# Kernel tuning notes

Hardware: AMD Instinct MI355X
Metric: run time of the kernel (lower is better)

## Reference

```python
import jax, jax.numpy as jnp
import numpy as np

D_MODEL = 1024
N_HEADS = 16
HEAD_DIM = D_MODEL // N_HEADS
B, S = 2, 2048


def setup_inputs() -> dict:
    key = jax.random.key(0)
    ks = jax.random.split(key, 6)
    w_scale = 1.0 / np.sqrt(D_MODEL)
    return {
        "query": jax.random.normal(ks[0], (B, S, D_MODEL), dtype=jnp.float32),
        "Wq": jax.random.normal(ks[1], (D_MODEL, D_MODEL), dtype=jnp.float32) * w_scale,
        "Wk": jax.random.normal(ks[2], (D_MODEL, D_MODEL), dtype=jnp.float32) * w_scale,
        "Wv": jax.random.normal(ks[3], (D_MODEL, D_MODEL), dtype=jnp.float32) * w_scale,
        "Wo": jax.random.normal(ks[4], (D_MODEL, D_MODEL), dtype=jnp.float32) * w_scale,
        "bo": jnp.zeros((D_MODEL,), dtype=jnp.float32),
    }


def reference(query, Wq, Wk, Wv, Wo, bo):
    # Self-attention: key = value = query (forward() defaults).
    b, t, _ = query.shape
    # Q/K/V projections (nn.Linear applies x @ W.T; weights here are stored as
    # [out, in] like torch, so project with W.T). Split into heads: [B,H,T,Dh].
    def proj(x, W):
        return (x @ W.T).reshape(b, t, N_HEADS, HEAD_DIM).transpose(0, 2, 1, 3)

    q = proj(query, Wq)
    k = proj(query, Wk)
    v = proj(query, Wv)

    scale = 1.0 / np.sqrt(HEAD_DIM)
    scores = jnp.einsum("bhqd,bhkd->bhqk", q, k) * scale  # [B,H,T,T]
    # Causal mask (is_causal=True, not cross-attention).
    causal = jnp.tril(jnp.ones((t, t), dtype=bool))
    scores = jnp.where(causal, scores, jnp.finfo(scores.dtype).min)
    weights = jax.nn.softmax(scores, axis=-1)
    out = jnp.einsum("bhqk,bhkd->bhqd", weights, v)  # [B,H,T,Dh]
    out = out.transpose(0, 2, 1, 3).reshape(b, t, D_MODEL)
    # Output projection with bias (dropout is identity in eval mode).
    return out @ Wo.T + bo
```

## Files before the change

### kernel.cpp

```cpp
#include <hip/hip_runtime.h>
#include <hip/hip_bf16.h>
#include <math.h>

typedef __attribute__((ext_vector_type(8))) short short8;
typedef __attribute__((ext_vector_type(4))) float floatx4;
typedef __attribute__((ext_vector_type(2))) _Float16 half2v;
typedef __attribute__((ext_vector_type(4))) _Float16 half4v;

#define MFMA_BF16_32(a, b, c) __builtin_amdgcn_mfma_f32_16x16x32_bf16(a, b, c, 0, 0, 0)
#define MFMA_F16_16(a, b, c) __builtin_amdgcn_mfma_f32_16x16x16f16(a, b, c, 0, 0, 0)

#define PIPE_BAR2() asm volatile("s_waitcnt vmcnt(2)\n\ts_barrier" ::: "memory")
#define PIPE_BAR0() asm volatile("s_waitcnt vmcnt(0)\n\ts_barrier" ::: "memory")

static constexpr int NH = 16;
static constexpr int Bb = 2;
static constexpr int Ss = 2048;
static constexpr int DM = 1024;

__device__ inline unsigned short f2bf(float f) {
    unsigned int u = __float_as_uint(f);
    u += 0x7fffu + ((u >> 16) & 1u);
    return (unsigned short)(u >> 16);
}

__device__ __forceinline__ half2v pkrtz(float a, float b) {
    return __builtin_bit_cast(half2v, __builtin_amdgcn_cvt_pkrtz(a, b));
}

__device__ __forceinline__ void gload_lds16(const unsigned short* g, unsigned short* l) {
    __builtin_amdgcn_global_load_lds(
        (const __attribute__((address_space(1))) unsigned int*)g,
        (__attribute__((address_space(3))) unsigned int*)l, 16, 0, 0);
}

__global__ void convert_all(const float* __restrict__ X, const float* __restrict__ w0,
                            const float* __restrict__ w1, const float* __restrict__ w2,
                            const float* __restrict__ w3, unsigned short* __restrict__ dstX,
                            unsigned short* __restrict__ dstW) {
    const int bid = blockIdx.x;
    const float* src;
    unsigned short* dst;
    int i;
    if (bid < 4096) {
        src = X; dst = dstX; i = bid * 256 + threadIdx.x;
    } else {
        const int w = (bid - 4096) >> 10;
        src = (w == 0) ? w0 : (w == 1) ? w1 : (w == 2) ? w2 : w3;
        dst = dstW + (size_t)w * 1048576;
        i = ((bid - 4096) & 1023) * 256 + threadIdx.x;
    }
    float4 v = ((const float4*)src)[i];
    ushort4 o;
    o.x = f2bf(v.x); o.y = f2bf(v.y); o.z = f2bf(v.z); o.w = f2bf(v.w);
    ((ushort4*)dst)[i] = o;
}

__global__ __launch_bounds__(256, 6) void gemm_qkv(const unsigned short* __restrict__ A,
                                                   const unsigned short* __restrict__ W,
                                                   unsigned short* __restrict__ Qp,
                                                   unsigned short* __restrict__ Kp,
                                                   unsigned short* __restrict__ Vt) {
    __shared__ __align__(16) unsigned short S[2][6144];
    const int K = 1024;
    const int tid = threadIdx.x;
    const int wave = tid >> 6, lane = tid & 63;
    const int quad = lane >> 4, l16 = lane & 15;
    const int wr = wave >> 1, wc = wave & 1;

    const int lin = blockIdx.x;
    const int xcd = lin & 7, slot = lin >> 3;
    const int bxt = (xcd & 3) * 16 + (slot & 15);
    const int by = (xcd >> 2) * 12 + (slot >> 4);
    const int bm = bxt * 64;
    const int bn = by * 128;

    const int srow = tid >> 2;
    const int scg = (tid & 3) ^ ((srow >> 1) & 3);
    const unsigned short* gA0 = A + (size_t)(bm + srow) * K + scg * 8;
    const unsigned short* gB0 = W + (size_t)(bn + srow) * K + scg * 8;

    auto stage = [&](int k0, int buf) {
        gload_lds16(gA0 + k0, &S[buf][wave * 512]);
        gload_lds16(gB0 + k0, &S[buf][2048 + wave * 512]);
        gload_lds16(gB0 + (size_t)64 * K + k0, &S[buf][4096 + wave * 512]);
    };

    floatx4 acc[2][4];
#pragma unroll
    for (int i = 0; i < 2; i++)
#pragma unroll
        for (int j = 0; j < 4; j++) acc[i][j] = (floatx4)0.0f;

    stage(0, 0);
    int buf = 0;
    for (int k0 = 0; k0 < K; k0 += 32) {
        __syncthreads();
        if (k0 + 32 < K) stage(k0 + 32, buf ^ 1);
        short8 af[2];
#pragma unroll
        for (int im = 0; im < 2; im++) {
            const int frow = wr * 32 + im * 16 + l16;
            af[im] = *(const short8*)&S[buf][frow * 32 + ((quad ^ ((frow >> 1) & 3)) * 8)];
        }
#pragma unroll
        for (int jn = 0; jn < 4; jn++) {
            const int frow = wc * 64 + jn * 16 + l16;
            short8 bf = *(const short8*)&S[buf][2048 + frow * 32 +
                                               ((quad ^ ((frow >> 1) & 3)) * 8)];
#pragma unroll
            for (int im = 0; im < 2; im++) acc[im][jn] = MFMA_BF16_32(af[im], bf, acc[im][jn]);
        }
        buf ^= 1;
    }
    __syncthreads();

    if (by < 16) {
        unsigned short* LB = &S[0][0];
        unsigned short* dst = (by < 8) ? Qp : Kp;
        const int nb = (by & 7) * 128;
        const float scale = (by < 8) ? 0.125f : 1.0f;
#pragma unroll
        for (int im = 0; im < 2; im++)
#pragma unroll
            for (int jn = 0; jn < 4; jn++) {
                const int row = wr * 32 + im * 16 + quad * 4;
                const int col = wc * 64 + jn * 16 + l16;
#pragma unroll
                for (int r = 0; r < 4; r++)
                    LB[(row + r) * 132 + col] = f2bf(acc[im][jn][r] * scale);
            }
        __syncthreads();
#pragma unroll
        for (int i = 0; i < 4; ++i) {
            const int flat = i * 256 + tid;
            const int row = flat >> 4, ch = flat & 15;
            short8 v = *(const short8*)&LB[row * 132 + ch * 8];
            *(short8*)&dst[(size_t)(bm + row) * 1024 + nb + ch * 8] = v;
        }
    } else {
        _Float16* LF = (_Float16*)&S[0][0];
        const int dbase = (by - 16) * 128;
        const int bI = bm >> 11, sbase = bm & 2047;
#pragma unroll
        for (int im = 0; im < 2; im++)
#pragma unroll
            for (int jn = 0; jn < 4; jn++) {
                const int d = wc * 64 + jn * 16 + l16;
                const int sl = wr * 32 + im * 16 + quad * 4;
                *(half2v*)&LF[d * 66 + sl] = pkrtz(acc[im][jn][0], acc[im][jn][1]);
                *(half2v*)&LF[d * 66 + sl + 2] = pkrtz(acc[im][jn][2], acc[im][jn][3]);
            }
        __syncthreads();
#pragma unroll
        for (int i = 0; i < 4; ++i) {
            const int flat = i * 256 + tid;
            const int dr = flat >> 3, ch = flat & 7;
            short8 v = *(const short8*)&LF[dr * 66 + ch * 8];
            const int d = dbase + dr;
            const int head = d >> 6, d64 = d & 63;
            *(short8*)&Vt[(((size_t)(bI * 16 + head)) * 64 + d64) * 2048 + sbase + ch * 8] = v;
        }
    }
}

__global__ __launch_bounds__(256) void gemm_out(const unsigned short* __restrict__ A,
                                                const unsigned short* __restrict__ Bm,
                                                float* __restrict__ C,
                                                const float* __restrict__ bias) {
    __shared__ __align__(16) unsigned short As[2][8192];
    __shared__ __align__(16) unsigned short Bs[2][4096];
    const int K = 1024;
    const int tid = threadIdx.x;
    const int wave = tid >> 6, lane = tid & 63;
    const int quad = lane >> 4, l16 = lane & 15;

    const int l = blockIdx.x;
    const int xcd = l & 7, slot = l >> 3;
    const int bx = (xcd & 3) * 8 + (slot & 7);
    const int by = (xcd >> 2) * 8 + (slot >> 3);
    const int bm = bx * 128, bn = by * 64;

    const int s0 = wave * 64 + lane;
    const int srow = s0 >> 2;
    const int scg = (s0 & 3) ^ ((srow >> 1) & 3);
    const unsigned short* gA0 = A + (size_t)(bm + srow) * K + scg * 8;
    const unsigned short* gB0 = Bm + (size_t)(bn + srow) * K + scg * 8;

    auto stage = [&](int k0, int buf) {
#pragma unroll
        for (int kh = 0; kh < 2; ++kh) {
            gload_lds16(gA0 + k0 + kh * 32, &As[buf][kh * 4096 + wave * 512]);
            gload_lds16(gA0 + (size_t)64 * K + k0 + kh * 32,
                        &As[buf][kh * 4096 + 2048 + wave * 512]);
            gload_lds16(gB0 + k0 + kh * 32, &Bs[buf][kh * 2048 + wave * 512]);
        }
    };

    floatx4 acc[2][4];
#pragma unroll
    for (int i = 0; i < 2; i++)
#pragma unroll
        for (int j = 0; j < 4; j++) acc[i][j] = (floatx4)0.0f;

    stage(0, 0);
    int buf = 0;
    for (int k0 = 0; k0 < K; k0 += 64) {
        __syncthreads();
        if (k0 + 64 < K) stage(k0 + 64, buf ^ 1);
#pragma unroll
        for (int kh = 0; kh < 2; ++kh) {
            const int abase = kh * 4096, bbase = kh * 2048;
            short8 af[2];
#pragma unroll
            for (int im = 0; im < 2; im++) {
                const int frow = wave * 32 + im * 16 + l16;
                af[im] = *(const short8*)&As[buf][abase + frow * 32 +
                                                  ((quad ^ ((frow >> 1) & 3)) * 8)];
            }
#pragma unroll
            for (int jn = 0; jn < 4; jn++) {
                const int frow = jn * 16 + l16;
                short8 bf = *(const short8*)&Bs[buf][bbase + frow * 32 +
                                                     ((quad ^ ((frow >> 1) & 3)) * 8)];
#pragma unroll
                for (int im = 0; im < 2; im++) acc[im][jn] = MFMA_BF16_32(af[im], bf, acc[im][jn]);
            }
        }
        buf ^= 1;
    }

#pragma unroll
    for (int im = 0; im < 2; im++) {
#pragma unroll
        for (int jn = 0; jn < 4; jn++) {
            const int row0 = bm + wave * 32 + im * 16 + quad * 4;
            const int colg = bn + jn * 16 + l16;
            const float bv = bias[colg];
#pragma unroll
            for (int r = 0; r < 4; r++)
                C[(size_t)(row0 + r) * 1024 + colg] = acc[im][jn][r] + bv;
        }
    }
}

__global__ __launch_bounds__(512, 4) void flash_attn(const unsigned short* __restrict__ Qp,
                                                     const unsigned short* __restrict__ Kp,
                                                     const _Float16* __restrict__ Vt,
                                                     unsigned short* __restrict__ Out) {
    __shared__ __align__(16) unsigned short Ks[3][4096];
    __shared__ __align__(16) _Float16 Vs[3][4096];
    const int lin = blockIdx.x;
    const int xcd = lin & 7, slot = lin >> 3;
    const int pair = xcd * 4 + ((slot >> 4) & 3);
    const int h = pair & 15, b = pair >> 4;
    const int qt0 = slot & 15;
    const int qt = ((slot >> 5) & 1) ? 15 - qt0 : qt0;

    const int tid = threadIdx.x, w = tid >> 6, lane = tid & 63;
    const int quad = lane >> 4, l16 = lane & 15;

    short8 qf[2];
    {
        const unsigned short* qa =
            Qp + ((size_t)(b * 2048 + qt * 128 + w * 16 + l16) << 10) + h * 64 + quad * 8;
        qf[0] = *(const short8*)qa;
        qf[1] = *(const short8*)(qa + 32);
    }

    const int t8 = tid >> 3;
    const int cg = (tid & 7) ^ (t8 & 7);
    const unsigned short* gK0 = Kp + ((size_t)(b * 2048 + t8) << 10) + h * 64 + cg * 8;
    const _Float16* gV0 = Vt + ((size_t)((b * 16 + h) * 64 + t8) << 11) + cg * 8;
    unsigned short* ldsK = &Ks[0][0] + w * 512;
    _Float16* ldsV = &Vs[0][0] + w * 512;

    auto stage = [&](int kt, int buf) {
        const size_t ko = (size_t)kt << 16;
        const size_t vo = (size_t)kt << 6;
        gload_lds16(gK0 + ko, ldsK + buf * 4096);
        gload_lds16((const unsigned short*)(gV0 + vo), (unsigned short*)(ldsV + buf * 4096));
    };

    const int ktEnd = 2 * qt + 1;
    const int myEnd = 2 * qt + (w >> 2);
    stage(0, 0);
    stage(1, 1);

    floatx4 acc[4];
#pragma unroll
    for (int dt = 0; dt < 4; dt++) acc[dt] = (floatx4)0.0f;
    float lsum = 0.0f;
    const int qloc = (w & 3) * 16 + l16;
    const int sw = l16 & 7;

    int buf = 0;
    for (int kt = 0; kt <= ktEnd; ++kt) {
        if (kt < ktEnd) { PIPE_BAR2(); } else { PIPE_BAR0(); }
        const int nbuf = (buf == 2) ? 0 : buf + 1;
        const int pbuf = (nbuf == 2) ? 0 : nbuf + 1;
        if (kt + 2 <= ktEnd) stage(kt + 2, pbuf);
        if (kt <= myEnd) {
            const bool diag = (kt == myEnd);
            const int scMax = diag ? (w & 3) : 3;
            const unsigned short* KB = &Ks[buf][0];
            const _Float16* VB = &Vs[buf][0];

#pragma unroll
            for (int sc = 0; sc < 4; ++sc) {
                if (sc <= scMax) {
                    const int rowk = sc * 16 + l16;
                    short8 kf0 = *(const short8*)&KB[rowk * 64 + ((quad ^ sw) * 8)];
                    short8 kf1 = *(const short8*)&KB[rowk * 64 + (((4 + quad) ^ sw) * 8)];

                    floatx4 s = MFMA_BF16_32(kf0, qf[0], (floatx4)(-2.0f));
                    s = MFMA_BF16_32(kf1, qf[1], s);
                    float ps[4];
#pragma unroll
                    for (int r = 0; r < 4; ++r) {
                        float e = __expf(s[r]);
                        if (diag && (sc * 16 + quad * 4 + r > qloc)) e = 0.0f;
                        ps[r] = e;
                    }
                    lsum += (ps[0] + ps[1]) + (ps[2] + ps[3]);
                    half4v p = __builtin_shufflevector(pkrtz(ps[0], ps[1]),
                                                       pkrtz(ps[2], ps[3]), 0, 1, 2, 3);

#pragma unroll
                    for (int dt = 0; dt < 4; ++dt) {
                        const int rowv = dt * 16 + l16;
                        const int cgv = ((sc * 2 + (quad >> 1)) ^ sw);
                        half4v vf = *(const half4v*)&VB[rowv * 64 + cgv * 8 + (quad & 1) * 4];
                        acc[dt] = MFMA_F16_16(vf, p, acc[dt]);
                    }
                }
            }
        }
        buf = nbuf;
    }

    lsum += __shfl_xor(lsum, 16);
    lsum += __shfl_xor(lsum, 32);
    const float inv = 1.0f / lsum;

    const size_t row = (size_t)(b * 2048 + qt * 128 + w * 16 + l16);
#pragma unroll
    for (int dt = 0; dt < 4; ++dt) {
        const int col = h * 64 + dt * 16 + quad * 4;
        ushort4 o;
        o.x = f2bf(acc[dt][0] * inv);
        o.y = f2bf(acc[dt][1] * inv);
        o.z = f2bf(acc[dt][2] * inv);
        o.w = f2bf(acc[dt][3] * inv);
        *(ushort4*)&Out[row * 1024 + col] = o;
    }
}

extern "C" void kernel_launch(void* const* d_in, const int* in_sizes, int n_in,
                              void* d_out, int out_size, void* d_ws, size_t ws_size,
                              hipStream_t stream) {
    const float* X  = (const float*)d_in[0];
    const float* Wq = (const float*)d_in[1];
    const float* Wk = (const float*)d_in[2];
    const float* Wv = (const float*)d_in[3];
    const float* Wo = (const float*)d_in[4];
    const float* bo = (const float*)d_in[5];

    unsigned short* ws = (unsigned short*)d_ws;
    unsigned short* Xb   = ws;
    unsigned short* W4   = ws + (size_t)4194304;
    unsigned short* Wob  = W4 + (size_t)3145728;
    unsigned short* Qp   = ws + (size_t)8388608;
    unsigned short* Kp   = ws + (size_t)12582912;
    unsigned short* Vt   = ws + (size_t)16777216;
    unsigned short* At   = ws + (size_t)20971520;

    convert_all<<<8192, 256, 0, stream>>>(X, Wq, Wk, Wv, Wo, Xb, W4);

    gemm_qkv<<<1536, 256, 0, stream>>>(Xb, W4, Qp, Kp, Vt);

    flash_attn<<<512, 512, 0, stream>>>(Qp, Kp, (const _Float16*)Vt, At);

    gemm_out<<<512, 256, 0, stream>>>(At, Wob, (float*)d_out, bo);
}
```

Measured before the change: 182.9 us.

## Triple-buffer QKV and output GEMM loads with two-stage-ahead prefetch

Both GEMM kernels move from double-buffered LDS staging to a three-buffer ring that prefetches two k-steps ahead. A fine-grained s_waitcnt vmcnt(3) plus barrier replaces __syncthreads, so one stage of loads can stay in flight while the current tile is consumed. gemm_out also drops its K-step from 64 to 32 so its shared-memory footprint stays bounded, and its occupancy hint is set to 4. The aim is to hide global-load latency better, at the cost of more LDS per block and a lower occupancy target for gemm_qkv (6 to 4).

Measured after the change: 184.8 us. No clear change (+1.0%).

```diff
diff --git a/kernel.cpp b/kernel.cpp
--- a/kernel.cpp
+++ b/kernel.cpp
@@ -12,6 +12,8 @@
 
 #define PIPE_BAR2() asm volatile("s_waitcnt vmcnt(2)\n\ts_barrier" ::: "memory")
 #define PIPE_BAR0() asm volatile("s_waitcnt vmcnt(0)\n\ts_barrier" ::: "memory")
+#define GEMM_BAR3() asm volatile("s_waitcnt vmcnt(3) lgkmcnt(0)\n\ts_barrier" ::: "memory")
+#define GEMM_BAR0() asm volatile("s_waitcnt vmcnt(0) lgkmcnt(0)\n\ts_barrier" ::: "memory")
 
 static constexpr int NH = 16;
 static constexpr int Bb = 2;
@@ -56,12 +58,12 @@
     ((ushort4*)dst)[i] = o;
 }
 
-__global__ __launch_bounds__(256, 6) void gemm_qkv(const unsigned short* __restrict__ A,
+__global__ __launch_bounds__(256, 4) void gemm_qkv(const unsigned short* __restrict__ A,
                                                    const unsigned short* __restrict__ W,
                                                    unsigned short* __restrict__ Qp,
                                                    unsigned short* __restrict__ Kp,
                                                    unsigned short* __restrict__ Vt) {
-    __shared__ __align__(16) unsigned short S[2][6144];
+    __shared__ __align__(16) unsigned short S[3][6144];
     const int K = 1024;
     const int tid = threadIdx.x;
     const int wave = tid >> 6, lane = tid & 63;
@@ -93,10 +95,13 @@
         for (int j = 0; j < 4; j++) acc[i][j] = (floatx4)0.0f;
 
     stage(0, 0);
+    stage(32, 1);
     int buf = 0;
     for (int k0 = 0; k0 < K; k0 += 32) {
-        __syncthreads();
-        if (k0 + 32 < K) stage(k0 + 32, buf ^ 1);
+        if (k0 + 32 < K) { GEMM_BAR3(); } else { GEMM_BAR0(); }
+        const int nbuf = (buf == 2) ? 0 : buf + 1;
+        const int pbuf = (nbuf == 2) ? 0 : nbuf + 1;
+        if (k0 + 64 < K) stage(k0 + 64, pbuf);
         short8 af[2];
 #pragma unroll
         for (int im = 0; im < 2; im++) {
@@ -111,7 +116,7 @@
 #pragma unroll
             for (int im = 0; im < 2; im++) acc[im][jn] = MFMA_BF16_32(af[im], bf, acc[im][jn]);
         }
-        buf ^= 1;
+        buf = nbuf;
     }
     __syncthreads();
 
@@ -164,12 +169,12 @@
     }
 }
 
-__global__ __launch_bounds__(256) void gemm_out(const unsigned short* __restrict__ A,
-                                                const unsigned short* __restrict__ Bm,
-                                                float* __restrict__ C,
-                                                const float* __restrict__ bias) {
-    __shared__ __align__(16) unsigned short As[2][8192];
-    __shared__ __align__(16) unsigned short Bs[2][4096];
+__global__ __launch_bounds__(256, 4) void gemm_out(const unsigned short* __restrict__ A,
+                                                   const unsigned short* __restrict__ Bm,
+                                                   float* __restrict__ C,
+                                                   const float* __restrict__ bias) {
+    __shared__ __align__(16) unsigned short As[3][4096];
+    __shared__ __align__(16) unsigned short Bs[3][2048];
     const int K = 1024;
     const int tid = threadIdx.x;
     const int wave = tid >> 6, lane = tid & 63;
@@ -181,20 +186,15 @@
     const int by = (xcd >> 2) * 8 + (slot >> 3);
     const int bm = bx * 128, bn = by * 64;
 
-    const int s0 = wave * 64 + lane;
-    const int srow = s0 >> 2;
-    const int scg = (s0 & 3) ^ ((srow >> 1) & 3);
+    const int srow = tid >> 2;
+    const int scg = (tid & 3) ^ ((srow >> 1) & 3);
     const unsigned short* gA0 = A + (size_t)(bm + srow) * K + scg * 8;
     const unsigned short* gB0 = Bm + (size_t)(bn + srow) * K + scg * 8;
 
     auto stage = [&](int k0, int buf) {
-#pragma unroll
-        for (int kh = 0; kh < 2; ++kh) {
-            gload_lds16(gA0 + k0 + kh * 32, &As[buf][kh * 4096 + wave * 512]);
-            gload_lds16(gA0 + (size_t)64 * K + k0 + kh * 32,
-                        &As[buf][kh * 4096 + 2048 + wave * 512]);
-            gload_lds16(gB0 + k0 + kh * 32, &Bs[buf][kh * 2048 + wave * 512]);
-        }
+        gload_lds16(gA0 + k0, &As[buf][wave * 512]);
+        gload_lds16(gA0 + (size_t)64 * K + k0, &As[buf][2048 + wave * 512]);
+        gload_lds16(gB0 + k0, &Bs[buf][wave * 512]);
     };
 
     floatx4 acc[2][4];
@@ -204,30 +204,27 @@
         for (int j = 0; j < 4; j++) acc[i][j] = (floatx4)0.0f;
 
     stage(0, 0);
+    stage(32, 1);
     int buf = 0;
-    for (int k0 = 0; k0 < K; k0 += 64) {
-        __syncthreads();
-        if (k0 + 64 < K) stage(k0 + 64, buf ^ 1);
-#pragma unroll
-        for (int kh = 0; kh < 2; ++kh) {
-            const int abase = kh * 4096, bbase = kh * 2048;
-            short8 af[2];
-#pragma unroll
-            for (int im = 0; im < 2; im++) {
-                const int frow = wave * 32 + im * 16 + l16;
-                af[im] = *(const short8*)&As[buf][abase + frow * 32 +
-                                                  ((quad ^ ((frow >> 1) & 3)) * 8)];
-            }
-#pragma unroll
-            for (int jn = 0; jn < 4; jn++) {
-                const int frow = jn * 16 + l16;
-                short8 bf = *(const short8*)&Bs[buf][bbase + frow * 32 +
-                                                     ((quad ^ ((frow >> 1) & 3)) * 8)];
-#pragma unroll
-                for (int im = 0; im < 2; im++) acc[im][jn] = MFMA_BF16_32(af[im], bf, acc[im][jn]);
-            }
-        }
-        buf ^= 1;
+    for (int k0 = 0; k0 < K; k0 += 32) {
+        if (k0 + 32 < K) { GEMM_BAR3(); } else { GEMM_BAR0(); }
+        const int nbuf = (buf == 2) ? 0 : buf + 1;
+        const int pbuf = (nbuf == 2) ? 0 : nbuf + 1;
+        if (k0 + 64 < K) stage(k0 + 64, pbuf);
+        short8 af[2];
+#pragma unroll
+        for (int im = 0; im < 2; im++) {
+            const int frow = wave * 32 + im * 16 + l16;
+            af[im] = *(const short8*)&As[buf][frow * 32 + ((quad ^ ((frow >> 1) & 3)) * 8)];
+        }
+#pragma unroll
+        for (int jn = 0; jn < 4; jn++) {
+            const int frow = jn * 16 + l16;
+            short8 bf = *(const short8*)&Bs[buf][frow * 32 + ((quad ^ ((frow >> 1) & 3)) * 8)];
+#pragma unroll
+            for (int im = 0; im < 2; im++) acc[im][jn] = MFMA_BF16_32(af[im], bf, acc[im][jn]);
+        }
+        buf = nbuf;
     }
 
 #pragma unroll
```
